# Performance work log

Measured on AMD Instinct MI355X. Metric: run time of the kernel, lower is better.

The kernel has to match this reference:

```python
import jax, jax.numpy as jnp
import numpy as np

N, K, D = 32768, 16, 128
EPS = 1e-5

def _bn(x, gamma, beta):
    # training-mode BatchNorm1d: biased batch stats over node axis
    mu = jnp.mean(x, axis=0, keepdims=True)
    var = jnp.mean((x - mu) ** 2, axis=0, keepdims=True)
    return gamma * (x - mu) / jnp.sqrt(var + EPS) + beta

def setup_inputs() -> dict:
    key = jax.random.key(0)
    ks = jax.random.split(key, 12)
    s = 0.02
    return {
        "h": jax.random.normal(ks[0], (N, D), jnp.float32),
        "neighbor_idx": jax.random.randint(ks[1], (N, K), 0, N, jnp.int32),
        # EdgeDistancesPassing MLP: Linear(D,D) -> ReLU -> Linear(D,1) -> ReLU
        "W1": jax.random.normal(ks[2], (D, D), jnp.float32) * s,
        "b1": jnp.zeros((D,), jnp.float32),
        "W2": jax.random.normal(ks[3], (D, 1), jnp.float32) * s,
        "b2": jnp.zeros((1,), jnp.float32),
        # MeanMax_aggregation O: Linear(2D, D)
        "OW": jax.random.normal(ks[4], (2 * D, D), jnp.float32) * s,
        "Ob": jnp.zeros((D,), jnp.float32),
        "bn1_g": jnp.ones((D,), jnp.float32),
        "bn1_b": jnp.zeros((D,), jnp.float32),
        # FFN
        "F1W": jax.random.normal(ks[5], (D, 2 * D), jnp.float32) * s,
        "F1b": jnp.zeros((2 * D,), jnp.float32),
        "F2W": jax.random.normal(ks[6], (2 * D, D), jnp.float32) * s,
        "F2b": jnp.zeros((D,), jnp.float32),
        "bn2_g": jnp.ones((D,), jnp.float32),
        "bn2_b": jnp.zeros((D,), jnp.float32),
    }

def reference(h, neighbor_idx, W1, b1, W2, b2, OW, Ob, bn1_g, bn1_b,
              F1W, F1b, F2W, F2b, bn2_g, bn2_b):
    # ---- EdgeDistancesPassing: per-edge MLP on (src - dst) features ----
    h_src = h[neighbor_idx]                      # [N, K, D] gather of source nodes
    dif = h_src - h[:, None, :]                  # edges.src - edges.dst
    a = jax.nn.relu(jnp.einsum('nkd,de->nke', dif, W1) + b1)
    att = jax.nn.relu(jnp.einsum('nkd,do->nko', a, W2) + b2)  # [N, K, 1]
    att = jnp.exp(-att)
    msg = att * h[:, None, :]                    # att_weight * edges.dst['features']
    # ---- MeanMax aggregation over mailbox (fixed in-degree K) ----
    mean_agg = jnp.mean(msg, axis=1)             # [N, D]
    max_agg = jnp.max(msg, axis=1)               # [N, D]
    out = jnp.concatenate([mean_agg, max_agg], axis=-1) @ OW + Ob
    # ---- residual + BN + FFN + residual + BN ----
    x = _bn(h + out, bn1_g, bn1_b)
    y = jax.nn.relu(x @ F1W + F1b) @ F2W + F2b
    return _bn(x + y, bn2_g, bn2_b)
```

## Files before the change

kernel.cpp:

```cpp
#include <hip/hip_runtime.h>
#include <math.h>

#define NN 32768
#define KK 16
#define DD 128
#define EPSV 1e-5f

typedef __attribute__((ext_vector_type(8))) short bf16x8;
typedef __attribute__((ext_vector_type(4))) float f32x4;

__device__ __forceinline__ unsigned short f2bf(float x) {
    unsigned u; __builtin_memcpy(&u, &x, 4);
    u += 0x7fffu + ((u >> 16) & 1u);
    return (unsigned short)(u >> 16);
}
__device__ __forceinline__ float bf2f(unsigned short b) {
    unsigned u = ((unsigned)b) << 16; float f; __builtin_memcpy(&f, &u, 4); return f;
}

#define MFMA16(a, b, c) __builtin_amdgcn_mfma_f32_16x16x32_bf16((a), (b), (c), 0, 0, 0)

__device__ __forceinline__ int swz(int row, int col) {
    return row * 128 + (col ^ ((row & 7) << 3));
}

__global__ __launch_bounds__(256) void k_prep_w4(const float* __restrict__ W1,
                                                 const float* __restrict__ OW,
                                                 const float* __restrict__ F1W,
                                                 const float* __restrict__ F2W,
                                                 short* __restrict__ w1b,
                                                 short* __restrict__ owb,
                                                 short* __restrict__ f1wb,
                                                 short* __restrict__ f2wb,
                                                 float* __restrict__ stats) {
    int tid = blockIdx.x * 256 + threadIdx.x;
    if (tid >= 14848) return;
    if (tid >= 14336) { stats[tid - 14336] = 0.f; return; }
    const float* W; short* out; int Ncol; int base;
    if (tid < 2048)       { W = W1;  out = w1b;  Ncol = 128; base = 0; }
    else if (tid < 6144)  { W = OW;  out = owb;  Ncol = 128; base = 2048; }
    else if (tid < 10240) { W = F1W; out = f1wb; Ncol = 256; base = 6144; }
    else                  { W = F2W; out = f2wb; Ncol = 128; base = 10240; }
    int t = tid - base;
    int l = t & 63, sc = t >> 6;
    int NT = Ncol >> 4;
    int c = sc % NT, s = sc / NT;
    int col = c * 16 + (l & 15);
    int k0 = s * 32 + (l >> 4) * 8;
    bf16x8 v;
    #pragma unroll
    for (int j = 0; j < 8; ++j) v[j] = (short)f2bf(W[(size_t)(k0 + j) * Ncol + col]);
    *(bf16x8*)(out + (size_t)t * 8) = v;
}

__global__ __launch_bounds__(512) void k_g(const float* __restrict__ h,
                                           const short* __restrict__ w1b,
                                           unsigned short* __restrict__ gb) {
    __shared__ unsigned short h_lds[64 * 128];
    const int t = threadIdx.x, w = t >> 6, l = t & 63;
    const int g16 = l >> 4, r16 = l & 15;
    const int rowb = blockIdx.x * 64;

    {
        int row = t >> 3, c0 = (t & 7) * 16;
        #pragma unroll
        for (int i = 0; i < 2; ++i) {
            int c = c0 + i * 8;
            const float* hp = h + (size_t)(rowb + row) * DD + c;
            float4 x0 = *(const float4*)hp;
            float4 x1 = *(const float4*)(hp + 4);
            bf16x8 hv;
            hv[0] = (short)f2bf(x0.x); hv[1] = (short)f2bf(x0.y);
            hv[2] = (short)f2bf(x0.z); hv[3] = (short)f2bf(x0.w);
            hv[4] = (short)f2bf(x1.x); hv[5] = (short)f2bf(x1.y);
            hv[6] = (short)f2bf(x1.z); hv[7] = (short)f2bf(x1.w);
            *(bf16x8*)&h_lds[swz(row, c)] = hv;
        }
    }
    __syncthreads();

    f32x4 acc[4];
    #pragma unroll
    for (int rt = 0; rt < 4; ++rt) acc[rt] = (f32x4){0.f, 0.f, 0.f, 0.f};
    #pragma unroll
    for (int s = 0; s < 4; ++s) {
        bf16x8 a[4];
        #pragma unroll
        for (int rt = 0; rt < 4; ++rt)
            a[rt] = *(const bf16x8*)&h_lds[swz(rt * 16 + r16, s * 32 + g16 * 8)];
        bf16x8 b = *(const bf16x8*)(w1b + ((size_t)(s * 8 + w) * 64 + l) * 8);
        #pragma unroll
        for (int rt = 0; rt < 4; ++rt) acc[rt] = MFMA16(a[rt], b, acc[rt]);
    }
    int col = w * 16 + r16;
    #pragma unroll
    for (int rt = 0; rt < 4; ++rt)
        #pragma unroll
        for (int j = 0; j < 4; ++j)
            gb[(size_t)(rowb + rt * 16 + g16 * 4 + j) * DD + col] = f2bf(acc[rt][j]);
}

__global__ __launch_bounds__(256) void k_att(const unsigned short* __restrict__ gb,
                                             const int* __restrict__ nbr,
                                             const float* __restrict__ b1,
                                             const float* __restrict__ W2,
                                             const float* __restrict__ b2,
                                             float* __restrict__ amean,
                                             float* __restrict__ amaxv,
                                             float* __restrict__ aminv) {
    const int t = threadIdx.x;
    const int w = t >> 6, lane = t & 63;
    const int node = blockIdx.x * 4 + w;
    const int grp = lane >> 4, r = lane & 15;

    bf16x8 gd8 = *(const bf16x8*)((const short*)gb + (size_t)node * DD + r * 8);
    float gd[8];
    #pragma unroll
    for (int j = 0; j < 8; ++j) gd[j] = bf2f((unsigned short)gd8[j]);
    float4 b1a = *(const float4*)(b1 + r * 8);
    float4 b1b = *(const float4*)(b1 + r * 8 + 4);
    float4 w2a = *(const float4*)(W2 + r * 8);
    float4 w2b = *(const float4*)(W2 + r * 8 + 4);
    const float b1v[8] = {b1a.x, b1a.y, b1a.z, b1a.w, b1b.x, b1b.y, b1b.z, b1b.w};
    const float w2v[8] = {w2a.x, w2a.y, w2a.z, w2a.w, w2b.x, w2b.y, w2b.z, w2b.w};
    const float b2s = b2[0];

    int4 nb4 = *(const int4*)(nbr + node * KK + grp * 4);
    const int srcs[4] = {nb4.x, nb4.y, nb4.z, nb4.w};

    float asum = 0.f, amx = -1e30f, amn = 1e30f;
    #pragma unroll
    for (int it = 0; it < 4; ++it) {
        bf16x8 gs8 = *(const bf16x8*)((const short*)gb + (size_t)srcs[it] * DD + r * 8);
        float v = 0.f;
        #pragma unroll
        for (int j = 0; j < 8; ++j)
            v += fmaxf(bf2f((unsigned short)gs8[j]) - gd[j] + b1v[j], 0.f) * w2v[j];
        v += __shfl_xor(v, 1); v += __shfl_xor(v, 2);
        v += __shfl_xor(v, 4); v += __shfl_xor(v, 8);
        float s = fmaxf(v + b2s, 0.f);
        float att = __expf(-s);
        asum += att;
        amx = fmaxf(amx, att);
        amn = fminf(amn, att);
    }
    asum += __shfl_xor(asum, 16); asum += __shfl_xor(asum, 32);
    amx = fmaxf(amx, __shfl_xor(amx, 16)); amx = fmaxf(amx, __shfl_xor(amx, 32));
    amn = fminf(amn, __shfl_xor(amn, 16)); amn = fminf(amn, __shfl_xor(amn, 32));
    if (lane == 0) {
        amean[node] = asum * (1.f / KK);
        amaxv[node] = amx;
        aminv[node] = amn;
    }
}

__global__ __launch_bounds__(512) void k_t(const short* __restrict__ owb,
                                           const float* __restrict__ h,
                                           const float* __restrict__ Ob,
                                           const float* __restrict__ amean,
                                           const float* __restrict__ amaxv,
                                           const float* __restrict__ aminv,
                                           unsigned short* __restrict__ tb,
                                           float* __restrict__ bnsum,
                                           float* __restrict__ bnsq) {
    __shared__ unsigned short aM_lds[64 * 128];
    __shared__ unsigned short aS_lds[64 * 128];
    const int t = threadIdx.x, w = t >> 6, l = t & 63;
    const int g16 = l >> 4, r16 = l & 15;
    const int rowb = blockIdx.x * 64;

    {
        int row = t >> 3, c0 = (t & 7) * 16;
        float am = amean[rowb + row], ax = amaxv[rowb + row], an = aminv[rowb + row];
        #pragma unroll
        for (int i = 0; i < 2; ++i) {
            int c = c0 + i * 8;
            const float* hp = h + (size_t)(rowb + row) * DD + c;
            float4 x0 = *(const float4*)hp;
            float4 x1 = *(const float4*)(hp + 4);
            float v[8] = {x0.x, x0.y, x0.z, x0.w, x1.x, x1.y, x1.z, x1.w};
            bf16x8 m, sfr;
            #pragma unroll
            for (int j = 0; j < 8; ++j) {
                m[j]   = (short)f2bf(am * v[j]);
                sfr[j] = (short)f2bf((v[j] >= 0.f ? ax : an) * v[j]);
            }
            *(bf16x8*)&aM_lds[swz(row, c)] = m;
            *(bf16x8*)&aS_lds[swz(row, c)] = sfr;
        }
    }
    __syncthreads();

    f32x4 acc[4];
    #pragma unroll
    for (int rt = 0; rt < 4; ++rt) acc[rt] = (f32x4){0.f, 0.f, 0.f, 0.f};
    #pragma unroll
    for (int s = 0; s < 4; ++s) {
        bf16x8 aM[4], aS[4];
        #pragma unroll
        for (int rt = 0; rt < 4; ++rt) {
            aM[rt] = *(const bf16x8*)&aM_lds[swz(rt * 16 + r16, s * 32 + g16 * 8)];
            aS[rt] = *(const bf16x8*)&aS_lds[swz(rt * 16 + r16, s * 32 + g16 * 8)];
        }
        bf16x8 bM = *(const bf16x8*)(owb + ((size_t)(s * 8 + w) * 64 + l) * 8);
        bf16x8 bS = *(const bf16x8*)(owb + ((size_t)((s + 4) * 8 + w) * 64 + l) * 8);
        #pragma unroll
        for (int rt = 0; rt < 4; ++rt) {
            acc[rt] = MFMA16(aM[rt], bM, acc[rt]);
            acc[rt] = MFMA16(aS[rt], bS, acc[rt]);
        }
    }

    {
        int col = w * 16 + r16;
        float ob = Ob[col];
        float cs = 0.f, cq = 0.f;
        #pragma unroll
        for (int rt = 0; rt < 4; ++rt)
            #pragma unroll
            for (int j = 0; j < 4; ++j) {
                int row = rowb + rt * 16 + g16 * 4 + j;
                size_t idx = (size_t)row * DD + col;
                float tv = h[idx] + acc[rt][j] + ob;
                tb[idx] = f2bf(tv);
                cs += tv; cq += tv * tv;
            }
        cs += __shfl_xor(cs, 16); cs += __shfl_xor(cs, 32);
        cq += __shfl_xor(cq, 16); cq += __shfl_xor(cq, 32);
        if (g16 == 0) {
            atomicAdd(&bnsum[col], cs);
            atomicAdd(&bnsq[col], cq);
        }
    }
}

__global__ __launch_bounds__(512) void k_ffn12(const unsigned short* __restrict__ tb,
                                               const short* __restrict__ f1wb,
                                               const float* __restrict__ F1b,
                                               const short* __restrict__ f2wb,
                                               const float* __restrict__ F2b,
                                               const float* __restrict__ bn1g,
                                               const float* __restrict__ bn1b,
                                               const float* __restrict__ bnsum1,
                                               const float* __restrict__ bnsq1,
                                               unsigned short* __restrict__ zb,
                                               float* __restrict__ bnsum2,
                                               float* __restrict__ bnsq2) {
    __shared__ unsigned short x_lds[64 * 128];
    __shared__ unsigned short u_lds[64 * 128];
    __shared__ float sc_l[128], sh_l[128];

    const int t = threadIdx.x, w = t >> 6, l = t & 63;
    const int g16 = l >> 4, r16 = l & 15;
    const int rowb = blockIdx.x * 64;
    const float inv = 1.f / NN;

    if (t < 128) {
        float mu = bnsum1[t] * inv;
        float var = bnsq1[t] * inv - mu * mu;
        float sc = bn1g[t] * rsqrtf(var + EPSV);
        sc_l[t] = sc;
        sh_l[t] = bn1b[t] - mu * sc;
    }
    __syncthreads();

    {
        int row = t >> 3, c0 = (t & 7) * 16;
        #pragma unroll
        for (int i = 0; i < 2; ++i) {
            int c = c0 + i * 8;
            bf16x8 v = *(const bf16x8*)(tb + (size_t)(rowb + row) * DD + c);
            bf16x8 xv;
            #pragma unroll
            for (int j = 0; j < 8; ++j)
                xv[j] = (short)f2bf(bf2f((unsigned short)v[j]) * sc_l[c + j] + sh_l[c + j]);
            *(bf16x8*)&x_lds[swz(row, c)] = xv;
        }
    }
    __syncthreads();

    f32x4 acc2[4];
    #pragma unroll
    for (int rt = 0; rt < 4; ++rt) acc2[rt] = (f32x4){0.f, 0.f, 0.f, 0.f};

    #pragma unroll 1
    for (int ct = 0; ct < 2; ++ct) {
        f32x4 acc1[4];
        #pragma unroll
        for (int rt = 0; rt < 4; ++rt) acc1[rt] = (f32x4){0.f, 0.f, 0.f, 0.f};
        #pragma unroll
        for (int s = 0; s < 4; ++s) {
            bf16x8 a[4];
            #pragma unroll
            for (int rt = 0; rt < 4; ++rt)
                a[rt] = *(const bf16x8*)&x_lds[swz(rt * 16 + r16, s * 32 + g16 * 8)];
            int fc = ct * 8 + w;
            bf16x8 b = *(const bf16x8*)(f1wb + ((size_t)(s * 16 + fc) * 64 + l) * 8);
            #pragma unroll
            for (int rt = 0; rt < 4; ++rt) acc1[rt] = MFMA16(a[rt], b, acc1[rt]);
        }
        {
            int colh = w * 16 + r16;
            float fb = F1b[ct * 128 + colh];
            #pragma unroll
            for (int rt = 0; rt < 4; ++rt)
                #pragma unroll
                for (int j = 0; j < 4; ++j)
                    u_lds[swz(rt * 16 + g16 * 4 + j, colh)] =
                        f2bf(fmaxf(acc1[rt][j] + fb, 0.f));
        }
        __syncthreads();
        #pragma unroll
        for (int ks = 0; ks < 4; ++ks) {
            bf16x8 a2[4];
            #pragma unroll
            for (int rt = 0; rt < 4; ++rt)
                a2[rt] = *(const bf16x8*)&u_lds[swz(rt * 16 + r16, ks * 32 + g16 * 8)];
            int sg = ct * 4 + ks;
            bf16x8 b = *(const bf16x8*)(f2wb + ((size_t)(sg * 8 + w) * 64 + l) * 8);
            #pragma unroll
            for (int rt = 0; rt < 4; ++rt) acc2[rt] = MFMA16(a2[rt], b, acc2[rt]);
        }
        __syncthreads();
    }

    {
        int col = w * 16 + r16;
        float fb = F2b[col];
        float cs = 0.f, cq = 0.f;
        #pragma unroll
        for (int rt = 0; rt < 4; ++rt)
            #pragma unroll
            for (int j = 0; j < 4; ++j) {
                int lr = rt * 16 + g16 * 4 + j;
                float xv = bf2f(x_lds[swz(lr, col)]);
                float zv = xv + acc2[rt][j] + fb;
                zb[(size_t)(rowb + lr) * DD + col] = f2bf(zv);
                cs += zv; cq += zv * zv;
            }
        cs += __shfl_xor(cs, 16); cs += __shfl_xor(cs, 32);
        cq += __shfl_xor(cq, 16); cq += __shfl_xor(cq, 32);
        if (g16 == 0) {
            atomicAdd(&bnsum2[col], cs);
            atomicAdd(&bnsq2[col], cq);
        }
    }
}

__global__ __launch_bounds__(256) void k_out(const unsigned short* __restrict__ zb,
                                             const float* __restrict__ bnsum,
                                             const float* __restrict__ bnsq,
                                             const float* __restrict__ gam,
                                             const float* __restrict__ bet,
                                             float* __restrict__ out) {
    int idx = blockIdx.x * 256 + threadIdx.x;
    int base = idx * 8;
    int c0 = base & 127;
    const float inv = 1.f / NN;
    bf16x8 zv = *(const bf16x8*)(zb + base);
    float o[8];
    #pragma unroll
    for (int j = 0; j < 8; ++j) {
        int c = c0 + j;
        float mu = bnsum[c] * inv;
        float var = bnsq[c] * inv - mu * mu;
        float sc = gam[c] * rsqrtf(var + EPSV);
        float sh = bet[c] - mu * sc;
        o[j] = bf2f((unsigned short)zv[j]) * sc + sh;
    }
    float4 o0 = {o[0], o[1], o[2], o[3]};
    float4 o1 = {o[4], o[5], o[6], o[7]};
    *(float4*)(out + base) = o0;
    *(float4*)(out + base + 4) = o1;
}

extern "C" void kernel_launch(void* const* d_in, const int* in_sizes, int n_in,
                              void* d_out, int out_size, void* d_ws, size_t ws_size,
                              hipStream_t stream) {
    const float* h    = (const float*)d_in[0];
    const int*   nbr  = (const int*)d_in[1];
    const float* W1   = (const float*)d_in[2];
    const float* b1   = (const float*)d_in[3];
    const float* W2   = (const float*)d_in[4];
    const float* b2   = (const float*)d_in[5];
    const float* OW   = (const float*)d_in[6];
    const float* Ob   = (const float*)d_in[7];
    const float* bn1g = (const float*)d_in[8];
    const float* bn1b = (const float*)d_in[9];
    const float* F1W  = (const float*)d_in[10];
    const float* F1b  = (const float*)d_in[11];
    const float* F2W  = (const float*)d_in[12];
    const float* F2b  = (const float*)d_in[13];
    const float* bn2g = (const float*)d_in[14];
    const float* bn2b = (const float*)d_in[15];
    float* out = (float*)d_out;

    char* wsb = (char*)d_ws;
    unsigned short* gb = (unsigned short*)wsb;
    unsigned short* tb = (unsigned short*)(wsb + ((size_t)8 << 20));
    unsigned short* zb = (unsigned short*)(wsb + ((size_t)16 << 20));
    char* wtb = wsb + ((size_t)24 << 20);
    short* w1b  = (short*)wtb;
    short* owb  = w1b + 16384;
    short* f1wb = owb + 32768;
    short* f2wb = f1wb + 32768;
    float* stats = (float*)(f2wb + 32768);
    float* bnsum1 = stats;
    float* bnsq1  = stats + 128;
    float* bnsum2 = stats + 256;
    float* bnsq2  = stats + 384;
    float* amean  = stats + 512;
    float* amaxv  = amean + NN;
    float* aminv  = amaxv + NN;

    k_prep_w4<<<58, 256, 0, stream>>>(W1, OW, F1W, F2W, w1b, owb, f1wb, f2wb, stats);
    k_g<<<NN / 64, 512, 0, stream>>>(h, w1b, gb);
    k_att<<<NN / 4, 256, 0, stream>>>(gb, nbr, b1, W2, b2, amean, amaxv, aminv);
    k_t<<<NN / 64, 512, 0, stream>>>((const short*)owb, h, Ob, amean, amaxv, aminv,
                                     tb, bnsum1, bnsq1);
    k_ffn12<<<NN / 64, 512, 0, stream>>>(tb, (const short*)f1wb, F1b,
                                         (const short*)f2wb, F2b, bn1g, bn1b,
                                         bnsum1, bnsq1, zb, bnsum2, bnsq2);
    k_out<<<NN * 16 / 256, 256, 0, stream>>>(zb, bnsum2, bnsq2, bn2g, bn2b, out);
}
```

Baseline: 79.67 us.

## Shrink prep kernel, fold weight conversion into k_g, and flatten FFN loop

The prep kernel now converts only W1 and zeroes the stats. The OW, F1W and F2W bf16 conversions move into 24 extra blocks appended to the k_g launch, so they run alongside the first GEMM instead of on the serial critical path. In k_ffn12 the two-chunk loop over the hidden dimension becomes one pass: the full 256-wide ReLU hidden tile is held in a doubled LDS buffer, which removes two block-wide barriers. The cost is more LDS per block, which may lower occupancy, and more accumulator registers.

```diff
diff --git a/kernel.cpp b/kernel.cpp
--- a/kernel.cpp
+++ b/kernel.cpp
@@ -23,39 +23,53 @@
 __device__ __forceinline__ int swz(int row, int col) {
     return row * 128 + (col ^ ((row & 7) << 3));
 }
-
-__global__ __launch_bounds__(256) void k_prep_w4(const float* __restrict__ W1,
-                                                 const float* __restrict__ OW,
-                                                 const float* __restrict__ F1W,
-                                                 const float* __restrict__ F2W,
-                                                 short* __restrict__ w1b,
-                                                 short* __restrict__ owb,
-                                                 short* __restrict__ f1wb,
-                                                 short* __restrict__ f2wb,
-                                                 float* __restrict__ stats) {
+__device__ __forceinline__ int swz256(int row, int col) {
+    return row * 256 + (col ^ ((row & 7) << 3));
+}
+
+__global__ __launch_bounds__(256) void k_prep(const float* __restrict__ W1,
+                                              short* __restrict__ w1b,
+                                              float* __restrict__ stats) {
     int tid = blockIdx.x * 256 + threadIdx.x;
-    if (tid >= 14848) return;
-    if (tid >= 14336) { stats[tid - 14336] = 0.f; return; }
-    const float* W; short* out; int Ncol; int base;
-    if (tid < 2048)       { W = W1;  out = w1b;  Ncol = 128; base = 0; }
-    else if (tid < 6144)  { W = OW;  out = owb;  Ncol = 128; base = 2048; }
-    else if (tid < 10240) { W = F1W; out = f1wb; Ncol = 256; base = 6144; }
-    else                  { W = F2W; out = f2wb; Ncol = 128; base = 10240; }
-    int t = tid - base;
-    int l = t & 63, sc = t >> 6;
-    int NT = Ncol >> 4;
-    int c = sc % NT, s = sc / NT;
+    if (tid >= 2560) return;
+    if (tid >= 2048) { stats[tid - 2048] = 0.f; return; }
+    int l = tid & 63, sc = tid >> 6;
+    int c = sc & 7, s = sc >> 3;
     int col = c * 16 + (l & 15);
     int k0 = s * 32 + (l >> 4) * 8;
     bf16x8 v;
     #pragma unroll
-    for (int j = 0; j < 8; ++j) v[j] = (short)f2bf(W[(size_t)(k0 + j) * Ncol + col]);
-    *(bf16x8*)(out + (size_t)t * 8) = v;
+    for (int j = 0; j < 8; ++j) v[j] = (short)f2bf(W1[(size_t)(k0 + j) * DD + col]);
+    *(bf16x8*)(w1b + (size_t)tid * 8) = v;
 }
 
 __global__ __launch_bounds__(512) void k_g(const float* __restrict__ h,
                                            const short* __restrict__ w1b,
-                                           unsigned short* __restrict__ gb) {
+                                           unsigned short* __restrict__ gb,
+                                           const float* __restrict__ OW,
+                                           const float* __restrict__ F1W,
+                                           const float* __restrict__ F2W,
+                                           short* __restrict__ owb,
+                                           short* __restrict__ f1wb,
+                                           short* __restrict__ f2wb) {
+    if (blockIdx.x >= NN / 64) {
+        int tid = (blockIdx.x - NN / 64) * 512 + threadIdx.x;
+        const float* W; short* out; int Ncol;
+        if (tid < 4096)      { W = OW;  out = owb;  Ncol = 128; }
+        else if (tid < 8192) { W = F1W; out = f1wb; Ncol = 256; tid -= 4096; }
+        else                 { W = F2W; out = f2wb; Ncol = 128; tid -= 8192; }
+        int l = tid & 63, sc = tid >> 6;
+        int NT = Ncol >> 4;
+        int c = sc % NT, s = sc / NT;
+        int col = c * 16 + (l & 15);
+        int k0 = s * 32 + (l >> 4) * 8;
+        bf16x8 v;
+        #pragma unroll
+        for (int j = 0; j < 8; ++j) v[j] = (short)f2bf(W[(size_t)(k0 + j) * Ncol + col]);
+        *(bf16x8*)(out + (size_t)tid * 8) = v;
+        return;
+    }
+
     __shared__ unsigned short h_lds[64 * 128];
     const int t = threadIdx.x, w = t >> 6, l = t & 63;
     const int g16 = l >> 4, r16 = l & 15;
@@ -247,7 +261,7 @@
                                                float* __restrict__ bnsum2,
                                                float* __restrict__ bnsq2) {
     __shared__ unsigned short x_lds[64 * 128];
-    __shared__ unsigned short u_lds[64 * 128];
+    __shared__ unsigned short u_lds[64 * 256];
     __shared__ float sc_l[128], sh_l[128];
 
     const int t = threadIdx.x, w = t >> 6, l = t & 63;
@@ -279,49 +293,50 @@
     }
     __syncthreads();
 
+    f32x4 acc1[4][2];
+    #pragma unroll
+    for (int rt = 0; rt < 4; ++rt)
+        #pragma unroll
+        for (int cc = 0; cc < 2; ++cc) acc1[rt][cc] = (f32x4){0.f, 0.f, 0.f, 0.f};
+    #pragma unroll
+    for (int s = 0; s < 4; ++s) {
+        bf16x8 a[4];
+        #pragma unroll
+        for (int rt = 0; rt < 4; ++rt)
+            a[rt] = *(const bf16x8*)&x_lds[swz(rt * 16 + r16, s * 32 + g16 * 8)];
+        #pragma unroll
+        for (int cc = 0; cc < 2; ++cc) {
+            int fc = cc * 8 + w;
+            bf16x8 b = *(const bf16x8*)(f1wb + ((size_t)(s * 16 + fc) * 64 + l) * 8);
+            #pragma unroll
+            for (int rt = 0; rt < 4; ++rt) acc1[rt][cc] = MFMA16(a[rt], b, acc1[rt][cc]);
+        }
+    }
+    #pragma unroll
+    for (int cc = 0; cc < 2; ++cc) {
+        int colu = (cc * 8 + w) * 16 + r16;
+        float fb = F1b[colu];
+        #pragma unroll
+        for (int rt = 0; rt < 4; ++rt)
+            #pragma unroll
+            for (int j = 0; j < 4; ++j)
+                u_lds[swz256(rt * 16 + g16 * 4 + j, colu)] =
+                    f2bf(fmaxf(acc1[rt][cc][j] + fb, 0.f));
+    }
+    __syncthreads();
+
     f32x4 acc2[4];
     #pragma unroll
     for (int rt = 0; rt < 4; ++rt) acc2[rt] = (f32x4){0.f, 0.f, 0.f, 0.f};
-
-    #pragma unroll 1
-    for (int ct = 0; ct < 2; ++ct) {
-        f32x4 acc1[4];
-        #pragma unroll
-        for (int rt = 0; rt < 4; ++rt) acc1[rt] = (f32x4){0.f, 0.f, 0.f, 0.f};
-        #pragma unroll
-        for (int s = 0; s < 4; ++s) {
-            bf16x8 a[4];
-            #pragma unroll
-            for (int rt = 0; rt < 4; ++rt)
-                a[rt] = *(const bf16x8*)&x_lds[swz(rt * 16 + r16, s * 32 + g16 * 8)];
-            int fc = ct * 8 + w;
-            bf16x8 b = *(const bf16x8*)(f1wb + ((size_t)(s * 16 + fc) * 64 + l) * 8);
-            #pragma unroll
-            for (int rt = 0; rt < 4; ++rt) acc1[rt] = MFMA16(a[rt], b, acc1[rt]);
-        }
-        {
-            int colh = w * 16 + r16;
-            float fb = F1b[ct * 128 + colh];
-            #pragma unroll
-            for (int rt = 0; rt < 4; ++rt)
-                #pragma unroll
-                for (int j = 0; j < 4; ++j)
-                    u_lds[swz(rt * 16 + g16 * 4 + j, colh)] =
-                        f2bf(fmaxf(acc1[rt][j] + fb, 0.f));
-        }
-        __syncthreads();
-        #pragma unroll
-        for (int ks = 0; ks < 4; ++ks) {
-            bf16x8 a2[4];
-            #pragma unroll
-            for (int rt = 0; rt < 4; ++rt)
-                a2[rt] = *(const bf16x8*)&u_lds[swz(rt * 16 + r16, ks * 32 + g16 * 8)];
-            int sg = ct * 4 + ks;
-            bf16x8 b = *(const bf16x8*)(f2wb + ((size_t)(sg * 8 + w) * 64 + l) * 8);
-            #pragma unroll
-            for (int rt = 0; rt < 4; ++rt) acc2[rt] = MFMA16(a2[rt], b, acc2[rt]);
-        }
-        __syncthreads();
+    #pragma unroll
+    for (int sg = 0; sg < 8; ++sg) {
+        bf16x8 a2[4];
+        #pragma unroll
+        for (int rt = 0; rt < 4; ++rt)
+            a2[rt] = *(const bf16x8*)&u_lds[swz256(rt * 16 + r16, sg * 32 + g16 * 8)];
+        bf16x8 b = *(const bf16x8*)(f2wb + ((size_t)(sg * 8 + w) * 64 + l) * 8);
+        #pragma unroll
+        for (int rt = 0; rt < 4; ++rt) acc2[rt] = MFMA16(a2[rt], b, acc2[rt]);
     }
 
     {
@@ -413,8 +428,8 @@
     float* amaxv  = amean + NN;
     float* aminv  = amaxv + NN;
 
-    k_prep_w4<<<58, 256, 0, stream>>>(W1, OW, F1W, F2W, w1b, owb, f1wb, f2wb, stats);
-    k_g<<<NN / 64, 512, 0, stream>>>(h, w1b, gb);
+    k_prep<<<10, 256, 0, stream>>>(W1, w1b, stats);
+    k_g<<<NN / 64 + 24, 512, 0, stream>>>(h, w1b, gb, OW, F1W, F2W, owb, f1wb, f2wb);
     k_att<<<NN / 4, 256, 0, stream>>>(gb, nbr, b1, W2, b2, amean, amaxv, aminv);
     k_t<<<NN / 64, 512, 0, stream>>>((const short*)owb, h, Ob, amean, amaxv, aminv,
                                      tb, bnsum1, bnsq1);
```

After: 78.61 us. No clear change (-1.3%).
